# Optimization experiments

Measured on AMD Instinct MI355X. Metric: run time of the kernel, lower is better.

Reference implementation:

```python
import jax, jax.numpy as jnp
import numpy as np
from jax import lax

B, T, N, H = 2048, 128, 128, 256  # batch, timesteps, input_size (drivers), hidden_size


def setup_inputs() -> dict:
    key = jax.random.key(0)
    k = jax.random.split(key, 7)
    s = 0.05
    return {
        "input_data": jax.random.normal(k[0], (B, T, N), jnp.float32),
        "w_ih": jax.random.normal(k[1], (4 * H, N), jnp.float32) * s,   # PyTorch weight_ih_l0
        "w_hh": jax.random.normal(k[2], (4 * H, H), jnp.float32) * s,   # PyTorch weight_hh_l0
        "b_ih": jax.random.normal(k[3], (4 * H,), jnp.float32) * s,
        "b_hh": jax.random.normal(k[4], (4 * H,), jnp.float32) * s,
        "w_attn": jax.random.normal(k[5], (2 * H + T,), jnp.float32) * s,  # attn_linear weight (out=1)
        "b_attn": jax.random.normal(k[6], (1,), jnp.float32) * s,
    }


def reference(input_data, w_ih, w_hh, b_ih, b_hh, w_attn, b_attn):
    b, t_steps, n = input_data.shape
    h_dim = w_hh.shape[1]
    # Split attention weight: [h | c | driver-series] parts of the concat feature.
    w_h = w_attn[:h_dim]
    w_c = w_attn[h_dim:2 * h_dim]
    w_x = w_attn[2 * h_dim:]
    # Driver-series contribution to attn logits is time-invariant: [B, N]
    precomp = jnp.einsum("btn,t->bn", input_data, w_x)
    bias = b_attn[0]
    gate_bias = b_ih + b_hh

    xs = jnp.transpose(input_data, (1, 0, 2))  # [T, B, N]

    def step(carry, x_t):
        h, c = carry  # [B, H] each
        # hidden/cell are broadcast identically across the N drivers -> scalar per batch
        s = h @ w_h + c @ w_c                       # [B]
        logits = s[:, None] + precomp + bias        # [B, N]
        attn = jax.nn.softmax(logits, axis=1)       # [B, N]
        wx = attn * x_t                             # weighted input, [B, N]
        # PyTorch LSTM cell: gates ordered i, f, g, o
        gates = wx @ w_ih.T + h @ w_hh.T + gate_bias  # [B, 4H]
        i, f, g, o = jnp.split(gates, 4, axis=1)
        c_new = jax.nn.sigmoid(f) * c + jax.nn.sigmoid(i) * jnp.tanh(g)
        h_new = jax.nn.sigmoid(o) * jnp.tanh(c_new)
        return (h_new, c_new), (wx, h_new)

    h0 = jnp.zeros((b, h_dim), input_data.dtype)
    c0 = jnp.zeros((b, h_dim), input_data.dtype)
    _, (ws, hs) = lax.scan(step, (h0, c0), xs)
    input_weighted = jnp.transpose(ws, (1, 0, 2))  # [B, T, N]
    input_encoded = jnp.transpose(hs, (1, 0, 2))   # [B, T, H]
    return input_weighted, input_encoded
```

## Files before the change

### kernel.cpp

```cpp
#include <hip/hip_runtime.h>
#include <hip/hip_bf16.h>


#define B_ 2048
#define T_ 128
#define N_ 128
#define H_ 256
#define RG_ 64

typedef float f32x4 __attribute__((ext_vector_type(4)));
typedef short bf16x8 __attribute__((ext_vector_type(8)));
typedef unsigned short u16;

__device__ __forceinline__ u16 f2bf(float f) {
  unsigned int u = __float_as_uint(f);
  u += 0x7fffu + ((u >> 16) & 1u);
  return (u16)(u >> 16);
}
__device__ __forceinline__ float sigm(float x) { return 1.f / (1.f + __expf(-x)); }
__device__ __forceinline__ float tanh_(float x) {
  float e = __expf(2.f * x);
  return 1.f - 2.f / (e + 1.f);
}

__device__ __forceinline__ bf16x8 ld16_dev(const u16* p) {
  bf16x8 v;
  asm volatile("global_load_dwordx4 %0, %1, off sc0 sc1" : "=v"(v) : "v"(p));
  return v;
}
__device__ __forceinline__ void st2_dev(u16* p, unsigned int v) {
  asm volatile("global_store_short %0, %1, off sc0 sc1" :: "v"(p), "v"(v));
}

__global__ __launch_bounds__(128) void attn_wx_kernel(
    const float* __restrict__ x, const float* __restrict__ w_attn,
    float* __restrict__ out0) {
  const int b = blockIdx.x;
  const int n = threadIdx.x;
  const float* xb = x + (size_t)b * (T_ * N_);
  __shared__ float red[N_];
  float xv[T_];
  float p = 0.f;
#pragma unroll
  for (int t = 0; t < T_; ++t) {
    xv[t] = xb[t * N_ + n];
    p += xv[t] * w_attn[2 * H_ + t];
  }
  red[n] = p;
  __syncthreads();
  float m = red[0];
  for (int i = 1; i < N_; ++i) m = fmaxf(m, red[i]);
  float e = __expf(p - m);
  __syncthreads();
  red[n] = e;
  __syncthreads();
  float s = 0.f;
  for (int i = 0; i < N_; ++i) s += red[i];
  const float a = e / s;
  float* ob = out0 + (size_t)b * (T_ * N_);
#pragma unroll
  for (int t = 0; t < T_; ++t) ob[t * N_ + n] = a * xv[t];
}

__global__ __launch_bounds__(256) void prepack_kernel(
    const float* __restrict__ w_ih, const float* __restrict__ w_hh,
    u16* __restrict__ wpk) {
  const int idx = blockIdx.x * 256 + threadIdx.x;
  const int j = idx & 7;
  const int l = (idx >> 3) & 63;
  const int rest = idx >> 9;
  const int kc = rest % 12;
  const int wq = rest / 12;
  const int q = wq & 3;
  const int g16 = wq >> 2;
  const int grow = q * H_ + g16 * 16 + (l & 15);
  const int k = kc * 32 + ((l >> 4) << 3) + j;
  const float v = (k < N_) ? w_ih[(size_t)grow * N_ + k]
                           : w_hh[(size_t)grow * H_ + (k - N_)];
  wpk[idx] = f2bf(v);
}

__global__ __launch_bounds__(256, 1) void lstm_kernel(
    const float* __restrict__ wx,
    const u16* __restrict__ wpk,
    const float* __restrict__ b_ih, const float* __restrict__ b_hh,
    float* __restrict__ out1,
    u16* __restrict__ hx,
    int* __restrict__ flags) {
  __shared__ u16 hsh[2][32][72];
  const int bid = blockIdx.x;
  const int rg = bid >> 2, cg = bid & 3;
  const int rb = rg * 32;
  const int tid  = threadIdx.x;
  const int w    = tid >> 6;
  const int lane = tid & 63;
  const int l15  = lane & 15;
  const int koff = (lane >> 4) << 3;
  const int g16  = cg * 4 + w;
  const int hcol = cg * 64 + w * 16 + l15;

  bf16x8 wfrag[4][12];
  {
    const u16* wp = wpk + (size_t)(g16 * 48) * 512 + (size_t)lane * 8;
#pragma unroll
    for (int q = 0; q < 4; ++q)
#pragma unroll
      for (int kc = 0; kc < 12; ++kc)
        wfrag[q][kc] = *(const bf16x8*)(wp + (size_t)(q * 12 + kc) * 512);
  }
  float bias[4];
#pragma unroll
  for (int q = 0; q < 4; ++q)
    bias[q] = b_ih[q * H_ + hcol] + b_hh[q * H_ + hcol];
  float creg[2][4] = {};

  int* fl = &flags[rg * 16];
  int* myflag = &flags[(rg * 4 + cg) * 4 + w];

  f32x4 pf[2][4][2];
#pragma unroll
  for (int mt = 0; mt < 2; ++mt)
#pragma unroll
    for (int kc = 0; kc < 4; ++kc) {
      const float* p = wx + (size_t)(rb + mt * 16 + l15) * (T_ * N_)
                          + kc * 32 + koff;
      pf[mt][kc][0] = *(const f32x4*)p;
      pf[mt][kc][1] = *(const f32x4*)(p + 4);
    }

  for (int t = 0; t < T_; ++t) {
    f32x4 acc[2][4];
#pragma unroll
    for (int mt = 0; mt < 2; ++mt)
#pragma unroll
      for (int q = 0; q < 4; ++q)
        acc[mt][q] = (f32x4){bias[q], bias[q], bias[q], bias[q]};

#pragma unroll
    for (int kc = 0; kc < 4; ++kc)
#pragma unroll
      for (int mt = 0; mt < 2; ++mt) {
        f32x4 x0 = pf[mt][kc][0], x1 = pf[mt][kc][1];
        bf16x8 a;
        a[0] = (short)f2bf(x0[0]); a[1] = (short)f2bf(x0[1]);
        a[2] = (short)f2bf(x0[2]); a[3] = (short)f2bf(x0[3]);
        a[4] = (short)f2bf(x1[0]); a[5] = (short)f2bf(x1[1]);
        a[6] = (short)f2bf(x1[2]); a[7] = (short)f2bf(x1[3]);
#pragma unroll
        for (int q = 0; q < 4; ++q)
          acc[mt][q] = __builtin_amdgcn_mfma_f32_16x16x32_bf16(a, wfrag[q][kc], acc[mt][q], 0, 0, 0);
      }
    if (t + 1 < T_) {
#pragma unroll
      for (int mt = 0; mt < 2; ++mt)
#pragma unroll
        for (int kc = 0; kc < 4; ++kc) {
          const float* p = wx + (size_t)(rb + mt * 16 + l15) * (T_ * N_)
                              + (size_t)(t + 1) * N_ + kc * 32 + koff;
          pf[mt][kc][0] = *(const f32x4*)p;
          pf[mt][kc][1] = *(const f32x4*)(p + 4);
        }
    }

    if (t > 0) {
      int mn;
      do {
        mn = 0x7fffffff;
#pragma unroll
        for (int i = 0; i < 16; ++i) {
          int v = __hip_atomic_load(&fl[i], __ATOMIC_RELAXED, __HIP_MEMORY_SCOPE_AGENT);
          mn = min(mn, v);
        }
      } while (mn < t);
      __builtin_amdgcn_sched_barrier(0);

      const u16* hxr = hx + (size_t)(t & 1) * (RG_ * 4 * 32 * 64)
                          + (size_t)rg * (4 * 32 * 64);
      bf16x8 ah[2][8];
#pragma unroll
      for (int mt = 0; mt < 2; ++mt)
#pragma unroll
        for (int kc2 = 0; kc2 < 8; ++kc2) {
          const int pc = kc2 >> 1, kcl = kc2 & 1;
          if (pc == cg)
            ah[mt][kc2] = *(const bf16x8*)&hsh[t & 1][mt * 16 + l15][kcl * 32 + koff];
          else
            ah[mt][kc2] = ld16_dev(hxr + (size_t)pc * 2048
                                   + (mt * 16 + l15) * 64 + kcl * 32 + koff);
        }
      asm volatile("s_waitcnt vmcnt(0)" ::: "memory");
      __builtin_amdgcn_sched_barrier(0);
#pragma unroll
      for (int kc2 = 0; kc2 < 8; ++kc2)
#pragma unroll
        for (int q = 0; q < 4; ++q)
#pragma unroll
          for (int mt = 0; mt < 2; ++mt)
            acc[mt][q] = __builtin_amdgcn_mfma_f32_16x16x32_bf16(ah[mt][kc2], wfrag[q][4 + kc2], acc[mt][q], 0, 0, 0);
    }

    u16* hxw = hx + (size_t)((t + 1) & 1) * (RG_ * 4 * 32 * 64)
                  + ((size_t)rg * 4 + cg) * (32 * 64);
#pragma unroll
    for (int mt = 0; mt < 2; ++mt)
#pragma unroll
      for (int rr = 0; rr < 4; ++rr) {
        const float gi = acc[mt][0][rr];
        const float gf = acc[mt][1][rr];
        const float gg = acc[mt][2][rr];
        const float go = acc[mt][3][rr];
        const float c = sigm(gf) * creg[mt][rr] + sigm(gi) * tanh_(gg);
        creg[mt][rr] = c;
        const float h = sigm(go) * tanh_(c);
        const int row = mt * 16 + ((lane >> 4) << 2) + rr;
        out1[(size_t)(rb + row) * (T_ * H_) + (size_t)t * H_ + hcol] = h;
        const u16 hb = f2bf(h);
        hsh[(t + 1) & 1][row][w * 16 + l15] = hb;
        st2_dev(hxw + row * 64 + w * 16 + l15, (unsigned int)hb);
      }
    asm volatile("s_waitcnt vmcnt(0)" ::: "memory");
    if (lane == 0)
      __hip_atomic_store(myflag, t + 1, __ATOMIC_RELAXED, __HIP_MEMORY_SCOPE_AGENT);
    __syncthreads();
  }
}

extern "C" void kernel_launch(void* const* d_in, const int* in_sizes, int n_in,
                              void* d_out, int out_size, void* d_ws, size_t ws_size,
                              hipStream_t stream) {
  const float* x      = (const float*)d_in[0];
  const float* w_ih   = (const float*)d_in[1];
  const float* w_hh   = (const float*)d_in[2];
  const float* b_ih   = (const float*)d_in[3];
  const float* b_hh   = (const float*)d_in[4];
  const float* w_attn = (const float*)d_in[5];

  float* out0 = (float*)d_out;
  float* out1 = out0 + (size_t)B_ * T_ * N_;

  int* flags = (int*)d_ws;
  u16* wpk   = (u16*)((char*)d_ws + 16384);
  u16* hx    = (u16*)((char*)d_ws + 16384 + 786432);

  hipMemsetAsync(d_ws, 0, RG_ * 4 * 4 * sizeof(int), stream);
  prepack_kernel<<<dim3(1536), dim3(256), 0, stream>>>(w_ih, w_hh, wpk);
  attn_wx_kernel<<<dim3(B_), dim3(N_), 0, stream>>>(x, w_attn, out0);
  lstm_kernel<<<dim3(256), dim3(256), 0, stream>>>(out0, wpk, b_ih, b_hh,
                                                   out1, hx, flags);
}
```

Before: 989.6 us.

## Store hidden state in MFMA fragment layout and poll packed byte flags

The global hidden-state exchange buffer is rearranged into MFMA A-fragment order. After a block barrier, each wave writes one 16-byte vector per lane, taken from LDS, instead of eight scattered 2-byte stores, and readers fetch contiguous fragments. The 16 per-row-group ready flags become bytes, so a single dwordx4 load polls all of them instead of 16 atomic loads. This shortens the per-timestep cross-block handoff on the serial critical path. In exchange, the LDS round-trip and the global store now sit after the barrier, and the byte flags limit the step count to 255.

```diff
diff --git a/kernel.cpp b/kernel.cpp
--- a/kernel.cpp
+++ b/kernel.cpp
@@ -11,6 +11,8 @@
 typedef float f32x4 __attribute__((ext_vector_type(4)));
 typedef short bf16x8 __attribute__((ext_vector_type(8)));
 typedef unsigned short u16;
+typedef unsigned int u32;
+typedef u32 u32x4 __attribute__((ext_vector_type(4)));
 
 __device__ __forceinline__ u16 f2bf(float f) {
   unsigned int u = __float_as_uint(f);
@@ -28,8 +30,17 @@
   asm volatile("global_load_dwordx4 %0, %1, off sc0 sc1" : "=v"(v) : "v"(p));
   return v;
 }
-__device__ __forceinline__ void st2_dev(u16* p, unsigned int v) {
-  asm volatile("global_store_short %0, %1, off sc0 sc1" :: "v"(p), "v"(v));
+__device__ __forceinline__ void st16_dev(u16* p, bf16x8 v) {
+  asm volatile("global_store_dwordx4 %0, %1, off sc0 sc1" :: "v"(p), "v"(v) : "memory");
+}
+__device__ __forceinline__ void st1_dev(unsigned char* p, u32 v) {
+  asm volatile("global_store_byte %0, %1, off sc0 sc1" :: "v"(p), "v"(v) : "memory");
+}
+__device__ __forceinline__ u32x4 ld_flags(const unsigned char* p) {
+  u32x4 f;
+  asm volatile("global_load_dwordx4 %0, %1, off sc0 sc1\n\ts_waitcnt vmcnt(0)"
+               : "=v"(f) : "v"(p) : "memory");
+  return f;
 }
 
 __global__ __launch_bounds__(128) void attn_wx_kernel(
@@ -86,7 +97,7 @@
     const float* __restrict__ b_ih, const float* __restrict__ b_hh,
     float* __restrict__ out1,
     u16* __restrict__ hx,
-    int* __restrict__ flags) {
+    unsigned char* __restrict__ flags) {
   __shared__ u16 hsh[2][32][72];
   const int bid = blockIdx.x;
   const int rg = bid >> 2, cg = bid & 3;
@@ -114,8 +125,9 @@
     bias[q] = b_ih[q * H_ + hcol] + b_hh[q * H_ + hcol];
   float creg[2][4] = {};
 
-  int* fl = &flags[rg * 16];
-  int* myflag = &flags[(rg * 4 + cg) * 4 + w];
+  unsigned char* flrow  = flags + rg * 16;
+  unsigned char* myflag = flrow + cg * 4 + w;
+  const int mtf = w >> 1, kclf = w & 1;
 
   f32x4 pf[2][4][2];
 #pragma unroll
@@ -163,19 +175,20 @@
     }
 
     if (t > 0) {
-      int mn;
-      do {
-        mn = 0x7fffffff;
-#pragma unroll
-        for (int i = 0; i < 16; ++i) {
-          int v = __hip_atomic_load(&fl[i], __ATOMIC_RELAXED, __HIP_MEMORY_SCOPE_AGENT);
-          mn = min(mn, v);
+      while (true) {
+        u32x4 f = ld_flags(flrow);
+        int ok = 1;
+#pragma unroll
+        for (int i = 0; i < 4; ++i) {
+          u32 v = f[i];
+          ok &= ((v & 255u) >= (u32)t) & (((v >> 8) & 255u) >= (u32)t) &
+                (((v >> 16) & 255u) >= (u32)t) & (((v >> 24) & 255u) >= (u32)t);
         }
-      } while (mn < t);
+        if (ok) break;
+      }
       __builtin_amdgcn_sched_barrier(0);
 
-      const u16* hxr = hx + (size_t)(t & 1) * (RG_ * 4 * 32 * 64)
-                          + (size_t)rg * (4 * 32 * 64);
+      const u16* hxr = hx + ((size_t)(t & 1) * RG_ + rg) * (4 * 4 * 512);
       bf16x8 ah[2][8];
 #pragma unroll
       for (int mt = 0; mt < 2; ++mt)
@@ -185,8 +198,8 @@
           if (pc == cg)
             ah[mt][kc2] = *(const bf16x8*)&hsh[t & 1][mt * 16 + l15][kcl * 32 + koff];
           else
-            ah[mt][kc2] = ld16_dev(hxr + (size_t)pc * 2048
-                                   + (mt * 16 + l15) * 64 + kcl * 32 + koff);
+            ah[mt][kc2] = ld16_dev(hxr + ((size_t)pc * 4 + (mt * 2 + kcl)) * 512
+                                       + (size_t)lane * 8);
         }
       asm volatile("s_waitcnt vmcnt(0)" ::: "memory");
       __builtin_amdgcn_sched_barrier(0);
@@ -199,8 +212,7 @@
             acc[mt][q] = __builtin_amdgcn_mfma_f32_16x16x32_bf16(ah[mt][kc2], wfrag[q][4 + kc2], acc[mt][q], 0, 0, 0);
     }
 
-    u16* hxw = hx + (size_t)((t + 1) & 1) * (RG_ * 4 * 32 * 64)
-                  + ((size_t)rg * 4 + cg) * (32 * 64);
+    const int nxt = (t + 1) & 1;
 #pragma unroll
     for (int mt = 0; mt < 2; ++mt)
 #pragma unroll
@@ -214,14 +226,18 @@
         const float h = sigm(go) * tanh_(c);
         const int row = mt * 16 + ((lane >> 4) << 2) + rr;
         out1[(size_t)(rb + row) * (T_ * H_) + (size_t)t * H_ + hcol] = h;
-        const u16 hb = f2bf(h);
-        hsh[(t + 1) & 1][row][w * 16 + l15] = hb;
-        st2_dev(hxw + row * 64 + w * 16 + l15, (unsigned int)hb);
+        hsh[nxt][row][w * 16 + l15] = f2bf(h);
       }
-    asm volatile("s_waitcnt vmcnt(0)" ::: "memory");
-    if (lane == 0)
-      __hip_atomic_store(myflag, t + 1, __ATOMIC_RELAXED, __HIP_MEMORY_SCOPE_AGENT);
     __syncthreads();
+
+    {
+      bf16x8 fv = *(const bf16x8*)&hsh[nxt][mtf * 16 + l15][kclf * 32 + koff];
+      u16* dst = hx + (((size_t)nxt * RG_ + rg) * 4 + cg) * (4 * 512)
+                    + (size_t)w * 512 + (size_t)lane * 8;
+      st16_dev(dst, fv);
+      asm volatile("s_waitcnt vmcnt(0)" ::: "memory");
+      if (lane == 0) st1_dev(myflag, (u32)(t + 1));
+    }
   }
 }
 
@@ -238,11 +254,11 @@
   float* out0 = (float*)d_out;
   float* out1 = out0 + (size_t)B_ * T_ * N_;
 
-  int* flags = (int*)d_ws;
-  u16* wpk   = (u16*)((char*)d_ws + 16384);
-  u16* hx    = (u16*)((char*)d_ws + 16384 + 786432);
-
-  hipMemsetAsync(d_ws, 0, RG_ * 4 * 4 * sizeof(int), stream);
+  unsigned char* flags = (unsigned char*)d_ws;
+  u16* wpk = (u16*)((char*)d_ws + 16384);
+  u16* hx  = (u16*)((char*)d_ws + 16384 + 786432);
+
+  hipMemsetAsync(d_ws, 0, RG_ * 16, stream);
   prepack_kernel<<<dim3(1536), dim3(256), 0, stream>>>(w_ih, w_hh, wpk);
   attn_wx_kernel<<<dim3(B_), dim3(N_), 0, stream>>>(x, w_attn, out0);
   lstm_kernel<<<dim3(256), dim3(256), 0, stream>>>(out0, wpk, b_ih, b_hh,
```

New measurement: 961.2 us. -2.9%, faster.
